# Kernel tuning notes

Measured on AMD Instinct MI355X. Metric: run time of the kernel, lower is better.

The kernel has to match this reference:

```python
import jax, jax.numpy as jnp
import numpy as np

B = 8          # batch of protein states
N = 20000      # num_nodes (atoms)
D = 640        # input_dim (latent per atom)
R = 2500       # number of residues (segments)
BINS = 10      # output_size_per_segment = (1, 10)
HID = 128      # decoder hidden dim
COND = 3       # conditioner_mode='X_ref' -> 3D reference coords
EPS = 1e-5     # BatchNorm1d eps


def _make_res_id():
    # ragged residue sizes cycling [6,8,10,8] -> exactly R residues, N atoms
    sizes = np.tile(np.array([6, 8, 10, 8], dtype=np.int64), R // 4)
    assert sizes.sum() == N
    return jnp.asarray(np.repeat(np.arange(R), sizes), dtype=jnp.int32)


def setup_inputs() -> dict:
    key = jax.random.key(0)
    ks = jax.random.split(key, 6)
    x = jax.random.normal(ks[0], (B * N, D), dtype=jnp.float32)
    conditioner = jax.random.normal(ks[1], (N, COND), dtype=jnp.float32)
    res_id = _make_res_id()  # [N] int32, sorted, atom -> residue
    W1 = jax.random.normal(ks[2], (BINS + COND, HID), dtype=jnp.float32) * 0.2
    b1 = jnp.zeros((HID,), jnp.float32)
    gamma = jnp.ones((HID,), jnp.float32)
    beta = jnp.zeros((HID,), jnp.float32)
    W2 = jax.random.normal(ks[3], (HID, 3), dtype=jnp.float32) * 0.1
    b2 = jnp.zeros((3,), jnp.float32)
    return {"x": x, "conditioner": conditioner, "res_id": res_id,
            "W1": W1, "b1": b1, "gamma": gamma, "beta": beta,
            "W2": W2, "b2": b2}


def reference(x, conditioner, res_id, W1, b1, gamma, beta, W2, b2):
    # x: [B*N, D] -> [B, N, D]
    x3 = x.reshape(B, N, D)

    # --- fused per-residue AdaptiveAvgPool2d((1,10)) ---
    # H-axis (atoms in residue) -> 1 : ragged segment mean via segment_sum
    counts = jax.ops.segment_sum(jnp.ones((N,), x.dtype), res_id,
                                 num_segments=R)                  # [R]
    seg_sum = jax.vmap(
        lambda xb: jax.ops.segment_sum(xb, res_id, num_segments=R)
    )(x3)                                                          # [B, R, D]
    seg_mean = seg_sum / counts[None, :, None]
    # W-axis: D -> 10 adaptive bins (exact since D % 10 == 0)
    pooled_latent = seg_mean.reshape(B, R, BINS, D // BINS).mean(-1)  # [B,R,10]

    # expand residue pooled vector back to its atoms, concat conditioner
    per_atom = pooled_latent[:, res_id, :]                        # [B, N, 10]
    cond = jnp.broadcast_to(conditioner[None], (B, N, COND))      # [B, N, 3]
    feat = jnp.concatenate([per_atom, cond], axis=-1).reshape(B * N, BINS + COND)

    # --- decoder MLP: Linear -> ReLU -> BatchNorm1d (train stats) -> Linear ---
    h = jax.nn.relu(feat @ W1 + b1)                               # [B*N, 128]
    mu = h.mean(axis=0)
    var = ((h - mu) ** 2).mean(axis=0)                            # biased, as torch BN
    hn = (h - mu) * jax.lax.rsqrt(var + EPS) * gamma + beta
    out = hn @ W2 + b2                                            # [B*N, 3]
    return out.reshape(B, N, 3)
```

## Files before the change

### kernel.cpp

```cpp
#include <hip/hip_runtime.h>

#define BB    8
#define NN    20000
#define DD    640
#define RR    2500
#define NBINS 10
#define HID   128
#define MTOT  (BB*NN)

__global__ void seg_bounds_kernel(const int* __restrict__ res_id,
                                  int* __restrict__ seg_start) {
    int r = blockIdx.x * blockDim.x + threadIdx.x;
    if (r > RR) return;
    if (r == RR) { seg_start[RR] = NN; return; }
    int lo = 0, hi = NN;
    while (lo < hi) {
        int mid = (lo + hi) >> 1;
        if (res_id[mid] < r) lo = mid + 1; else hi = mid;
    }
    seg_start[r] = lo;
}

__global__ __launch_bounds__(640) void pool_kernel(const float* __restrict__ x,
                                                   const int* __restrict__ seg_start,
                                                   float* __restrict__ pooled) {
    int br = blockIdx.x;
    int b = br / RR;
    int r = br - b * RR;
    int t = threadIdx.x;
    int lane = t & 63;
    int wave = t >> 6;

    int s0  = seg_start[r];
    int cnt = seg_start[r + 1] - s0;

    const float* xp = x + ((size_t)(b * NN + s0)) * DD + t;
    float a0 = 0.f, a1 = 0.f;
    int a = 0;
    for (; a + 1 < cnt; a += 2) {
        a0 += xp[(size_t)a * DD];
        a1 += xp[(size_t)(a + 1) * DD];
    }
    if (a < cnt) a0 += xp[(size_t)a * DD];
    float sum = a0 + a1;

    #pragma unroll
    for (int o = 32; o > 0; o >>= 1) sum += __shfl_down(sum, o, 64);

    if (lane == 0) {
        float inv = cnt > 0 ? 1.f / (64.f * (float)cnt) : 0.f;
        pooled[(size_t)(b * RR + r) * NBINS + wave] = sum * inv;
    }
}

__global__ __launch_bounds__(128) void stats_kernel(const float* __restrict__ pooled,
                                                    const float* __restrict__ cond,
                                                    const int* __restrict__ res_id,
                                                    const float* __restrict__ W1,
                                                    const float* __restrict__ b1,
                                                    float* __restrict__ partial) {
    int k = threadIdx.x;
    float w[13];
    #pragma unroll
    for (int j = 0; j < 13; j++) w[j] = W1[j * HID + k];
    float bk = b1[k];

    float s = 0.f, s2 = 0.f;
    for (int i = blockIdx.x; i < MTOT; i += gridDim.x) {
        int b = i / NN;
        int n = i - b * NN;
        int rid = res_id[n];
        const float* pr = pooled + (size_t)(b * RR + rid) * NBINS;
        const float* cr = cond + (size_t)n * 3;
        float h = bk;
        #pragma unroll
        for (int j = 0; j < NBINS; j++) h = fmaf(pr[j], w[j], h);
        h = fmaf(cr[0], w[10], h);
        h = fmaf(cr[1], w[11], h);
        h = fmaf(cr[2], w[12], h);
        h = fmaxf(h, 0.f);
        s += h;
        s2 = fmaf(h, h, s2);
    }
    partial[blockIdx.x * 256 + k]       = s;
    partial[blockIdx.x * 256 + 128 + k] = s2;
}

__global__ __launch_bounds__(1024) void finalize_kernel(const float* __restrict__ partial,
                                                        const float* __restrict__ gamma,
                                                        const float* __restrict__ beta,
                                                        const float* __restrict__ W2,
                                                        const float* __restrict__ b2,
                                                        float* __restrict__ W2eff,
                                                        float* __restrict__ b2eff) {
    int t = threadIdx.x;
    int slot = t & 255;
    int grp  = t >> 8;
    float acc = 0.f;
    for (int bi = grp; bi < 1024; bi += 4) acc += partial[bi * 256 + slot];

    __shared__ float part4[4][256];
    __shared__ float contrib[HID * 3];
    part4[grp][slot] = acc;
    __syncthreads();

    if (t < HID) {
        float s  = part4[0][t] + part4[1][t] + part4[2][t] + part4[3][t];
        float s2 = part4[0][128 + t] + part4[1][128 + t] + part4[2][128 + t] + part4[3][128 + t];
        const float invM = 1.f / (float)MTOT;
        float mu  = s * invM;
        float var = fmaxf(s2 * invM - mu * mu, 0.f);
        float rs  = rsqrtf(var + 1e-5f);
        float sc  = gamma[t] * rs;
        float tk  = beta[t] - mu * sc;
        #pragma unroll
        for (int j = 0; j < 3; j++) {
            float wv = W2[t * 3 + j];
            W2eff[t * 3 + j]   = sc * wv;
            contrib[t * 3 + j] = tk * wv;
        }
    }
    __syncthreads();
    if (t < 3) {
        float a2 = b2[t];
        for (int kk = 0; kk < HID; kk++) a2 += contrib[kk * 3 + t];
        b2eff[t] = a2;
    }
}

__global__ __launch_bounds__(256) void out_kernel(const float* __restrict__ pooled,
                                                  const float* __restrict__ cond,
                                                  const int* __restrict__ res_id,
                                                  const float* __restrict__ W1,
                                                  const float* __restrict__ b1,
                                                  const float* __restrict__ W2eff,
                                                  const float* __restrict__ b2eff,
                                                  float* __restrict__ out) {
    int lane = threadIdx.x & 63;
    int wid  = (blockIdx.x * blockDim.x + threadIdx.x) >> 6;
    int nw   = (gridDim.x * blockDim.x) >> 6;
    int k1 = lane, k2 = lane + 64;

    float wa[13], wb[13];
    #pragma unroll
    for (int j = 0; j < 13; j++) {
        wa[j] = W1[j * HID + k1];
        wb[j] = W1[j * HID + k2];
    }
    float b1a = b1[k1], b1b = b1[k2];
    float wa0 = W2eff[k1 * 3 + 0], wa1 = W2eff[k1 * 3 + 1], wa2 = W2eff[k1 * 3 + 2];
    float wb0 = W2eff[k2 * 3 + 0], wb1 = W2eff[k2 * 3 + 1], wb2 = W2eff[k2 * 3 + 2];
    float e0 = b2eff[0], e1 = b2eff[1], e2 = b2eff[2];

    for (int i = wid; i < MTOT; i += nw) {
        int b = i / NN;
        int n = i - b * NN;
        int rid = res_id[n];
        const float* pr = pooled + (size_t)(b * RR + rid) * NBINS;
        const float* cr = cond + (size_t)n * 3;

        float h1 = b1a, h2 = b1b;
        #pragma unroll
        for (int j = 0; j < NBINS; j++) {
            h1 = fmaf(pr[j], wa[j], h1);
            h2 = fmaf(pr[j], wb[j], h2);
        }
        h1 = fmaf(cr[0], wa[10], h1); h1 = fmaf(cr[1], wa[11], h1); h1 = fmaf(cr[2], wa[12], h1);
        h2 = fmaf(cr[0], wb[10], h2); h2 = fmaf(cr[1], wb[11], h2); h2 = fmaf(cr[2], wb[12], h2);
        h1 = fmaxf(h1, 0.f);
        h2 = fmaxf(h2, 0.f);

        float p0 = h1 * wa0 + h2 * wb0;
        float p1 = h1 * wa1 + h2 * wb1;
        float p2 = h1 * wa2 + h2 * wb2;
        #pragma unroll
        for (int m = 1; m < 64; m <<= 1) {
            p0 += __shfl_xor(p0, m, 64);
            p1 += __shfl_xor(p1, m, 64);
            p2 += __shfl_xor(p2, m, 64);
        }
        if (lane == 0) {
            out[(size_t)i * 3 + 0] = p0 + e0;
            out[(size_t)i * 3 + 1] = p1 + e1;
            out[(size_t)i * 3 + 2] = p2 + e2;
        }
    }
}

extern "C" void kernel_launch(void* const* d_in, const int* in_sizes, int n_in,
                              void* d_out, int out_size, void* d_ws, size_t ws_size,
                              hipStream_t stream) {
    const float* x      = (const float*)d_in[0];
    const float* cond   = (const float*)d_in[1];
    const int*   res_id = (const int*)  d_in[2];
    const float* W1     = (const float*)d_in[3];
    const float* b1     = (const float*)d_in[4];
    const float* gamma  = (const float*)d_in[5];
    const float* beta   = (const float*)d_in[6];
    const float* W2     = (const float*)d_in[7];
    const float* b2     = (const float*)d_in[8];
    float* out = (float*)d_out;

    char* w = (char*)d_ws;
    int*   seg_start = (int*)  (w);
    float* pooled    = (float*)(w + 16384);
    float* partial   = (float*)(w + (1 << 20));
    float* W2eff     = (float*)(w + (2 << 20));
    float* b2eff     = (float*)(w + (2 << 20) + 4096);

    hipLaunchKernelGGL(seg_bounds_kernel, dim3(10), dim3(256), 0, stream,
                       res_id, seg_start);
    hipLaunchKernelGGL(pool_kernel, dim3(BB * RR), dim3(640), 0, stream,
                       x, seg_start, pooled);
    hipLaunchKernelGGL(stats_kernel, dim3(1024), dim3(128), 0, stream,
                       pooled, cond, res_id, W1, b1, partial);
    hipLaunchKernelGGL(finalize_kernel, dim3(1), dim3(1024), 0, stream,
                       partial, gamma, beta, W2, b2, W2eff, b2eff);
    hipLaunchKernelGGL(out_kernel, dim3(512), dim3(256), 0, stream,
                       pooled, cond, res_id, W1, b1, W2eff, b2eff, out);
}
```

Baseline: 784.6 us.

## Vectorize segment pooling with float4 loads and raise stats/output grid sizes

The pooling kernel now reads each residue's contiguous atom rows as float4 over a flat index, reduces across 16-lane groups, and accumulates the per-bin partial sums through shared-memory atomics. This is meant to raise memory throughput on the dominant 409 MB read of x. Separately, the stats and output kernels get twice as many blocks, and the workspace offsets are moved so the larger partial buffer fits. The shared atomics add some contention and change the order of the floating-point summation.

```diff
diff --git a/kernel.cpp b/kernel.cpp
--- a/kernel.cpp
+++ b/kernel.cpp
@@ -7,6 +7,7 @@
 #define NBINS 10
 #define HID   128
 #define MTOT  (BB*NN)
+#define SBLK  2048
 
 __global__ void seg_bounds_kernel(const int* __restrict__ res_id,
                                   int* __restrict__ seg_start) {
@@ -24,32 +25,37 @@
 __global__ __launch_bounds__(640) void pool_kernel(const float* __restrict__ x,
                                                    const int* __restrict__ seg_start,
                                                    float* __restrict__ pooled) {
+    __shared__ float sbin[NBINS];
     int br = blockIdx.x;
     int b = br / RR;
     int r = br - b * RR;
     int t = threadIdx.x;
-    int lane = t & 63;
-    int wave = t >> 6;
+    if (t < NBINS) sbin[t] = 0.f;
+    __syncthreads();
 
     int s0  = seg_start[r];
     int cnt = seg_start[r + 1] - s0;
-
-    const float* xp = x + ((size_t)(b * NN + s0)) * DD + t;
-    float a0 = 0.f, a1 = 0.f;
-    int a = 0;
-    for (; a + 1 < cnt; a += 2) {
-        a0 += xp[(size_t)a * DD];
-        a1 += xp[(size_t)(a + 1) * DD];
-    }
-    if (a < cnt) a0 += xp[(size_t)a * DD];
-    float sum = a0 + a1;
-
-    #pragma unroll
-    for (int o = 32; o > 0; o >>= 1) sum += __shfl_down(sum, o, 64);
-
-    if (lane == 0) {
+    int nf4 = (cnt * DD) >> 2;
+    const float4* xp = (const float4*)(x + (size_t)(b * NN + s0) * DD);
+
+    float sum = 0.f;
+    for (int idx = t; idx < nf4; idx += 640) {
+        float4 v = xp[idx];
+        sum += (v.x + v.y) + (v.z + v.w);
+    }
+
+    sum += __shfl_down(sum, 8, 16);
+    sum += __shfl_down(sum, 4, 16);
+    sum += __shfl_down(sum, 2, 16);
+    sum += __shfl_down(sum, 1, 16);
+    if ((t & 15) == 0) {
+        int bin = ((t << 2) % DD) >> 6;
+        atomicAdd(&sbin[bin], sum);
+    }
+    __syncthreads();
+    if (t < NBINS) {
         float inv = cnt > 0 ? 1.f / (64.f * (float)cnt) : 0.f;
-        pooled[(size_t)(b * RR + r) * NBINS + wave] = sum * inv;
+        pooled[(size_t)(b * RR + r) * NBINS + t] = sbin[t] * inv;
     }
 }
 
@@ -66,7 +72,7 @@
     float bk = b1[k];
 
     float s = 0.f, s2 = 0.f;
-    for (int i = blockIdx.x; i < MTOT; i += gridDim.x) {
+    for (int i = blockIdx.x; i < MTOT; i += SBLK) {
         int b = i / NN;
         int n = i - b * NN;
         int rid = res_id[n];
@@ -97,7 +103,7 @@
     int slot = t & 255;
     int grp  = t >> 8;
     float acc = 0.f;
-    for (int bi = grp; bi < 1024; bi += 4) acc += partial[bi * 256 + slot];
+    for (int bi = grp; bi < SBLK; bi += 4) acc += partial[bi * 256 + slot];
 
     __shared__ float part4[4][256];
     __shared__ float contrib[HID * 3];
@@ -205,17 +211,17 @@
     int*   seg_start = (int*)  (w);
     float* pooled    = (float*)(w + 16384);
     float* partial   = (float*)(w + (1 << 20));
-    float* W2eff     = (float*)(w + (2 << 20));
-    float* b2eff     = (float*)(w + (2 << 20) + 4096);
+    float* W2eff     = (float*)(w + (3 << 20));
+    float* b2eff     = (float*)(w + (3 << 20) + 4096);
 
     hipLaunchKernelGGL(seg_bounds_kernel, dim3(10), dim3(256), 0, stream,
                        res_id, seg_start);
     hipLaunchKernelGGL(pool_kernel, dim3(BB * RR), dim3(640), 0, stream,
                        x, seg_start, pooled);
-    hipLaunchKernelGGL(stats_kernel, dim3(1024), dim3(128), 0, stream,
+    hipLaunchKernelGGL(stats_kernel, dim3(SBLK), dim3(128), 0, stream,
                        pooled, cond, res_id, W1, b1, partial);
     hipLaunchKernelGGL(finalize_kernel, dim3(1), dim3(1024), 0, stream,
                        partial, gamma, beta, W2, b2, W2eff, b2eff);
-    hipLaunchKernelGGL(out_kernel, dim3(512), dim3(256), 0, stream,
+    hipLaunchKernelGGL(out_kernel, dim3(1024), dim3(256), 0, stream,
                        pooled, cond, res_id, W1, b1, W2eff, b2eff, out);
 }
```

Measured after the change: 784.5 us. No clear change (-0.0%).
